# Kernel tuning notes

Measured on AMD Instinct MI355X. Metric: run time of the kernel, lower is better.

## Reference

```python
import jax, jax.numpy as jnp
import numpy as np

N = 8192
D = 1024
TIME_DECAY = 86400.0
EPS = 1e-10


def setup_inputs() -> dict:
    key = jax.random.key(0)
    ks = jax.random.split(key, 8)
    x = jax.random.normal(ks[0], (N, D), dtype=jnp.float32)
    # timestamps spanning ~10 days so decay bias is non-trivial
    timestamps = jax.random.uniform(ks[1], (N,), dtype=jnp.float32) * (10.0 * TIME_DECAY)
    s = 1.0 / np.sqrt(D)
    Wq = jax.random.normal(ks[2], (D, D), dtype=jnp.float32) * s
    bq = jnp.zeros((D,), dtype=jnp.float32)
    Wk = jax.random.normal(ks[3], (D, D), dtype=jnp.float32) * s
    bk = jnp.zeros((D,), dtype=jnp.float32)
    Wv = jax.random.normal(ks[4], (D, D), dtype=jnp.float32) * s
    bv = jnp.zeros((D,), dtype=jnp.float32)
    return {"x": x, "timestamps": timestamps, "Wq": Wq, "bq": bq,
            "Wk": Wk, "bk": bk, "Wv": Wv, "bv": bv}


def reference(x, timestamps, Wq, bq, Wk, bk, Wv, bv):
    scale = jnp.asarray(D ** 0.5, x.dtype)
    # torch nn.Linear: y = x @ W.T + b
    Q = x @ Wq.T + bq          # [N, D]
    K = x @ Wk.T + bk          # [N, D]
    V = x @ Wv.T + bv          # [N, D]
    time_diff = timestamps[:, None] - timestamps[None, :]   # [N, N]
    time_decay = jnp.exp(-jnp.abs(time_diff) / TIME_DECAY)  # [N, N]
    scores = (Q @ K.T) / scale + jnp.log(time_decay + EPS)  # [N, N]
    attn = jax.nn.softmax(scores, axis=-1)
    return attn @ V
```

## Files before the change

kernel.cpp:

```cpp
#include <hip/hip_runtime.h>


using half8   = __attribute__((ext_vector_type(8))) _Float16;
using half4   = __attribute__((ext_vector_type(4))) _Float16;
using floatx4 = __attribute__((ext_vector_type(4))) float;

__device__ __forceinline__ void gload_lds16(const void* g, void* l) {
  __builtin_amdgcn_global_load_lds((const __attribute__((address_space(1))) void*)g,
                                   (__attribute__((address_space(3))) void*)l,
                                   16, 0, 0);
}

template<int BIAS_MODE, int OUT_MODE, int SWZ>
__global__ __launch_bounds__(256)
void gemm64_k(const _Float16* __restrict__ A, const _Float16* __restrict__ B,
              void* __restrict__ Cout, const float* __restrict__ bias,
              int lda, int ldb, int ldc, int K, float outScale)
{
  __shared__ __align__(16) _Float16 As[128 * 64];
  __shared__ __align__(16) _Float16 Bs[128 * 64];
  const int tid = threadIdx.x;
  const int w = tid >> 6, lane = tid & 63;
  const int q = lane >> 4, l15 = lane & 15;
  const int wr = w >> 1, wc = w & 1;

  int tx, ty;
  if (SWZ) {
    const int bflat = blockIdx.y * gridDim.x + blockIdx.x;
    ty = bflat % gridDim.y;
    tx = bflat / gridDim.y;
  } else {
    tx = blockIdx.x; ty = blockIdx.y;
  }
  const long rowBase = (long)ty * 128;
  const long colBase = (long)tx * 128;

  const _Float16* Ag[4]; const _Float16* Bg[4];
  _Float16* Al[4]; _Float16* Bl[4];
#pragma unroll
  for (int p = 0; p < 4; ++p) {
    const int e = w * 2048 + p * 512 + lane * 8;
    const int row = e >> 6, c = (e >> 3) & 7;
    const int sc = (c ^ (row & 7)) << 3;
    Ag[p] = A + (rowBase + row) * lda + sc;
    Bg[p] = B + (colBase + row) * ldb + sc;
    Al[p] = &As[w * 2048 + p * 512];
    Bl[p] = &Bs[w * 2048 + p * 512];
  }

  floatx4 acc[4][4] = {};

  for (int k0 = 0; k0 < K; k0 += 64) {
    __syncthreads();
#pragma unroll
    for (int p = 0; p < 4; ++p) {
      gload_lds16(Ag[p], Al[p]);
      gload_lds16(Bg[p], Bl[p]);
      Ag[p] += 64; Bg[p] += 64;
    }
    __syncthreads();
#pragma unroll
    for (int kk = 0; kk < 2; ++kk) {
      half8 b[4];
#pragma unroll
      for (int j = 0; j < 4; ++j) {
        const int R = wc * 64 + 16 * j + l15;
        b[j] = *(const half8*)&Bs[R * 64 + (((kk * 4 + q) ^ (R & 7)) << 3)];
      }
#pragma unroll
      for (int i = 0; i < 4; ++i) {
        const int R = wr * 64 + 16 * i + l15;
        const half8 a = *(const half8*)&As[R * 64 + (((kk * 4 + q) ^ (R & 7)) << 3)];
#pragma unroll
        for (int j = 0; j < 4; ++j)
          acc[i][j] = __builtin_amdgcn_mfma_f32_16x16x32_f16(a, b[j], acc[i][j], 0, 0, 0);
      }
    }
  }

#pragma unroll
  for (int i = 0; i < 4; ++i) {
#pragma unroll
    for (int r = 0; r < 4; ++r) {
      const long rowg = rowBase + wr * 64 + 16 * i + q * 4 + r;
#pragma unroll
      for (int j = 0; j < 4; ++j) {
        const long colg = colBase + wc * 64 + 16 * j + l15;
        float v = acc[i][j][r];
        if (BIAS_MODE == 1) v += bias[colg];
        if (BIAS_MODE == 2) v += bias[rowg];
        if (BIAS_MODE == 3) v *= bias[rowg];
        v *= outScale;
        if (OUT_MODE == 2) ((float*)Cout)[rowg * ldc + colg] = v;
        else               ((_Float16*)Cout)[rowg * ldc + colg] = (_Float16)v;
      }
    }
  }
}

__global__ __launch_bounds__(256)
void gemm_stats_k(const _Float16* __restrict__ A, const _Float16* __restrict__ B,
                  const float* __restrict__ ts, _Float16* __restrict__ U,
                  float* __restrict__ part, int lda, int ldb, int N, int K,
                  float qkScale)
{
  __shared__ __align__(16) _Float16 As[128 * 64];
  __shared__ __align__(16) _Float16 Bs[128 * 64];
  __shared__ float trs[128], tcs[128];
  __shared__ float sL[2][2][64];
  const int tid = threadIdx.x;
  const int w = tid >> 6, lane = tid & 63;
  const int q = lane >> 4, l15 = lane & 15;
  const int wr = w >> 1, wc = w & 1;
  const long rowBase = (long)blockIdx.y * 128;
  const long colBase = (long)blockIdx.x * 128;

  if (tid < 128) {
    trs[tid] = ts[rowBase + tid];
    tcs[tid] = ts[colBase + tid];
  }

  const _Float16* Ag[4]; const _Float16* Bg[4];
  _Float16* Al[4]; _Float16* Bl[4];
#pragma unroll
  for (int p = 0; p < 4; ++p) {
    const int e = w * 2048 + p * 512 + lane * 8;
    const int row = e >> 6, c = (e >> 3) & 7;
    const int sc = (c ^ (row & 7)) << 3;
    Ag[p] = A + (rowBase + row) * lda + sc;
    Bg[p] = B + (colBase + row) * ldb + sc;
    Al[p] = &As[w * 2048 + p * 512];
    Bl[p] = &Bs[w * 2048 + p * 512];
  }

  floatx4 acc[4][4] = {};

  for (int k0 = 0; k0 < K; k0 += 64) {
    __syncthreads();
#pragma unroll
    for (int p = 0; p < 4; ++p) {
      gload_lds16(Ag[p], Al[p]);
      gload_lds16(Bg[p], Bl[p]);
      Ag[p] += 64; Bg[p] += 64;
    }
    __syncthreads();
#pragma unroll
    for (int kk = 0; kk < 2; ++kk) {
      half8 b[4];
#pragma unroll
      for (int j = 0; j < 4; ++j) {
        const int R = wc * 64 + 16 * j + l15;
        b[j] = *(const half8*)&Bs[R * 64 + (((kk * 4 + q) ^ (R & 7)) << 3)];
      }
#pragma unroll
      for (int i = 0; i < 4; ++i) {
        const int R = wr * 64 + 16 * i + l15;
        const half8 a = *(const half8*)&As[R * 64 + (((kk * 4 + q) ^ (R & 7)) << 3)];
#pragma unroll
        for (int j = 0; j < 4; ++j)
          acc[i][j] = __builtin_amdgcn_mfma_f32_16x16x32_f16(a, b[j], acc[i][j], 0, 0, 0);
      }
    }
  }

  const float inv_td = 1.0f / 86400.0f;
#pragma unroll
  for (int i = 0; i < 4; ++i) {
#pragma unroll
    for (int r = 0; r < 4; ++r) {
      const int rowl = wr * 64 + 16 * i + q * 4 + r;
      float ls = 0.0f;
#pragma unroll
      for (int j = 0; j < 4; ++j) {
        const int coll = wc * 64 + 16 * j + l15;
        const float sv = acc[i][j][r] * qkScale
                       - fabsf(trs[rowl] - tcs[coll]) * inv_td - 4.0f;
        const float u = __expf(sv);
        ls += u;
        U[(rowBase + rowl) * (long)N + (colBase + coll)] = (_Float16)u;
      }
      for (int mask = 1; mask <= 8; mask <<= 1)
        ls += __shfl_xor(ls, mask, 64);
      if (l15 == 0) sL[wr][wc][16 * i + 4 * q + r] = ls;
    }
  }
  __syncthreads();
  if (tid < 128) {
    const int wr2 = tid >> 6, rl = tid & 63;
    part[(rowBase + tid) * 64 + blockIdx.x] = sL[wr2][0][rl] + sL[wr2][1][rl];
  }
}

__global__ void combine_k(const float* __restrict__ part, float* __restrict__ invL) {
  const int r = blockIdx.x * 256 + threadIdx.x;
  float L = 0.0f;
  for (int c = 0; c < 64; ++c) L += part[(long)r * 64 + c];
  invL[r] = 1.0f / L;
}

__global__ void cvt_k(const float* __restrict__ in, _Float16* __restrict__ out, int n) {
  const int i = (blockIdx.x * 256 + threadIdx.x) * 4;
  if (i >= n) return;
  const float4 v = *(const float4*)(in + i);
  half4 o = { (_Float16)v.x, (_Float16)v.y, (_Float16)v.z, (_Float16)v.w };
  *(half4*)(out + i) = o;
}

extern "C" void kernel_launch(void* const* d_in, const int* in_sizes, int n_in,
                              void* d_out, int out_size, void* d_ws, size_t ws_size,
                              hipStream_t stream)
{
  (void)in_sizes; (void)n_in; (void)out_size; (void)ws_size;
  const int N = 8192, D = 1024;
  const float* x  = (const float*)d_in[0];
  const float* ts = (const float*)d_in[1];
  const float* Wq = (const float*)d_in[2];
  const float* bq = (const float*)d_in[3];
  const float* Wk = (const float*)d_in[4];
  const float* bk = (const float*)d_in[5];
  const float* Wv = (const float*)d_in[6];
  const float* bv = (const float*)d_in[7];

  char* p = (char*)d_ws;
  auto grab = [&](size_t bytes) {
    char* r = p;
    p += (bytes + 255) & ~(size_t)255;
    return r;
  };
  _Float16* xh    = (_Float16*)grab((size_t)N * D * 2);
  _Float16* wqkh  = (_Float16*)grab((size_t)2 * D * D * 2);
  _Float16* wvh   = (_Float16*)grab((size_t)D * D * 2);
  _Float16* QKcat = (_Float16*)grab((size_t)N * 2 * D * 2);
  _Float16* VTh   = (_Float16*)grab((size_t)D * N * 2);
  _Float16* Uh    = (_Float16*)grab((size_t)N * N * 2);
  float*    part  = (float*)grab((size_t)N * 64 * sizeof(float));
  float*    invL  = (float*)grab((size_t)N * sizeof(float));
  float*    bcat  = (float*)grab((size_t)2 * D * sizeof(float));

  cvt_k<<<N * D / 1024, 256, 0, stream>>>(x,  xh,  N * D);
  cvt_k<<<D * D / 1024, 256, 0, stream>>>(Wq, wqkh,         D * D);
  cvt_k<<<D * D / 1024, 256, 0, stream>>>(Wk, wqkh + D * D, D * D);
  cvt_k<<<D * D / 1024, 256, 0, stream>>>(Wv, wvh, D * D);
  hipMemcpyAsync(bcat,     bq, D * sizeof(float), hipMemcpyDeviceToDevice, stream);
  hipMemcpyAsync(bcat + D, bk, D * sizeof(float), hipMemcpyDeviceToDevice, stream);

  dim3 blk(256);
  gemm64_k<1, 0, 0><<<dim3(2 * D / 128, N / 128), blk, 0, stream>>>(
      xh, wqkh, QKcat, bcat, D, D, 2 * D, D, 1.0f);
  gemm64_k<2, 0, 0><<<dim3(N / 128, D / 128), blk, 0, stream>>>(
      wvh, xh, VTh, bv, D, D, N, D, 1.0f);
  gemm_stats_k<<<dim3(N / 128, N / 128), blk, 0, stream>>>(
      QKcat, QKcat + D, ts, Uh, part, 2 * D, 2 * D, N, D, 1.0f / 32.0f);
  combine_k<<<N / 256, 256, 0, stream>>>(part, invL);
  gemm64_k<3, 2, 1><<<dim3(D / 128, N / 128), blk, 0, stream>>>(
      Uh, VTh, d_out, invL, N, N, D, N, 1.0f);
}
```

Baseline: 513.9 us.

## Replace GEMMs with 256-tile, 512-thread kernels using a 4-stage LDS ring

All GEMM kernels are rewritten around a shared k-loop that keeps a 4-slot LDS ring of 32-wide K slices. Each step issues loads three slices ahead and waits with explicit vmcnt counts plus raw barriers, so global-to-LDS traffic overlaps MFMA work. Tiles grow to 256x256 or 256x128 with 8 waves per block, and MFMA sections are raised with setprio. The stats kernel uses 256x256 tiles, which halves the partial-sum columns consumed by combine_k. The trade-off is higher register and LDS pressure, fewer blocks per grid, and hand-counted waitcnt synchronisation that can go wrong.

```diff
diff --git a/kernel.cpp b/kernel.cpp
--- a/kernel.cpp
+++ b/kernel.cpp
@@ -11,18 +11,104 @@
                                    16, 0, 0);
 }
 
-template<int BIAS_MODE, int OUT_MODE, int SWZ>
-__global__ __launch_bounds__(256)
-void gemm64_k(const _Float16* __restrict__ A, const _Float16* __restrict__ B,
-              void* __restrict__ Cout, const float* __restrict__ bias,
-              int lda, int ldb, int ldc, int K, float outScale)
-{
-  __shared__ __align__(16) _Float16 As[128 * 64];
-  __shared__ __align__(16) _Float16 Bs[128 * 64];
+template<int N> __device__ __forceinline__ void waitv() {
+  if constexpr (N == 12)      asm volatile("s_waitcnt vmcnt(12)" ::: "memory");
+  else if constexpr (N == 9)  asm volatile("s_waitcnt vmcnt(9)"  ::: "memory");
+  else if constexpr (N == 8)  asm volatile("s_waitcnt vmcnt(8)"  ::: "memory");
+  else if constexpr (N == 6)  asm volatile("s_waitcnt vmcnt(6)"  ::: "memory");
+  else if constexpr (N == 4)  asm volatile("s_waitcnt vmcnt(4)"  ::: "memory");
+  else if constexpr (N == 3)  asm volatile("s_waitcnt vmcnt(3)"  ::: "memory");
+  else                        asm volatile("s_waitcnt vmcnt(0)"  ::: "memory");
+}
+
+template<int BM, int BN, int WM, int WN, int MI, int NJ>
+__device__ __forceinline__ void kloop_ring(
+    const _Float16* __restrict__ A, const _Float16* __restrict__ B,
+    long rowBase, long colBase, int lda, int ldb, int K,
+    _Float16* __restrict__ As, _Float16* __restrict__ Bs,
+    floatx4 (&acc)[MI][NJ])
+{
+  constexpr int LA = BM / 128, LB = BN / 128;
+  constexpr int ISS = LA + LB;
   const int tid = threadIdx.x;
   const int w = tid >> 6, lane = tid & 63;
   const int q = lane >> 4, l15 = lane & 15;
-  const int wr = w >> 1, wc = w & 1;
+  const int wr = w / WN, wcn = w & (WN - 1);
+
+  const int sc = (((lane & 3) ^ ((lane >> 3) & 3)) << 3);
+  const _Float16* Agp[LA]; int Aoff[LA];
+  const _Float16* Bgp[LB]; int Boff[LB];
+#pragma unroll
+  for (int p = 0; p < LA; ++p) {
+    const int row = ((w * (BM * 4) + p * 512 + lane * 8) >> 5);
+    Agp[p] = A + (rowBase + row) * (long)lda + sc;
+    Aoff[p] = w * (BM * 4) + p * 512;
+  }
+#pragma unroll
+  for (int p = 0; p < LB; ++p) {
+    const int row = ((w * (BN * 4) + p * 512 + lane * 8) >> 5);
+    Bgp[p] = B + (colBase + row) * (long)ldb + sc;
+    Boff[p] = w * (BN * 4) + p * 512;
+  }
+
+  const int pRd   = (q ^ ((l15 >> 1) & 3)) << 3;
+  const int aBase = (wr * (BM / WM) + l15) * 32 + pRd;
+  const int bBase = (wcn * (BN / WN) + l15) * 32 + pRd;
+
+  auto issue = [&](int t) {
+    const int s = t & 3;
+    const long ko = (long)t * 32;
+    _Float16* Asl = As + s * (BM * 32);
+    _Float16* Bsl = Bs + s * (BN * 32);
+#pragma unroll
+    for (int p = 0; p < LA; ++p) gload_lds16(Agp[p] + ko, Asl + Aoff[p]);
+#pragma unroll
+    for (int p = 0; p < LB; ++p) gload_lds16(Bgp[p] + ko, Bsl + Boff[p]);
+  };
+
+  auto compute = [&](int slot) {
+    const _Float16* Asl = As + slot * (BM * 32);
+    const _Float16* Bsl = Bs + slot * (BN * 32);
+    half8 bfr[NJ], afr[MI];
+#pragma unroll
+    for (int j = 0; j < NJ; ++j) bfr[j] = *(const half8*)&Bsl[bBase + j * 512];
+#pragma unroll
+    for (int i = 0; i < MI; ++i) afr[i] = *(const half8*)&Asl[aBase + i * 512];
+    __builtin_amdgcn_s_setprio(1);
+#pragma unroll
+    for (int i = 0; i < MI; ++i)
+#pragma unroll
+      for (int j = 0; j < NJ; ++j)
+        acc[i][j] = __builtin_amdgcn_mfma_f32_16x16x32_f16(afr[i], bfr[j], acc[i][j], 0, 0, 0);
+    __builtin_amdgcn_s_setprio(0);
+  };
+
+  const int NT = K >> 5;
+  issue(0); issue(1); issue(2);
+  for (int t = 0; t < NT - 3; ++t) {
+    issue(t + 3);
+    waitv<3 * ISS>();
+    __builtin_amdgcn_s_barrier();
+    compute(t & 3);
+    __builtin_amdgcn_s_barrier();
+  }
+  waitv<2 * ISS>(); __builtin_amdgcn_s_barrier();
+  compute((NT - 3) & 3);          __builtin_amdgcn_s_barrier();
+  waitv<1 * ISS>(); __builtin_amdgcn_s_barrier();
+  compute((NT - 2) & 3);          __builtin_amdgcn_s_barrier();
+  waitv<0>();       __builtin_amdgcn_s_barrier();
+  compute((NT - 1) & 3);
+}
+
+template<int BM, int BN, int WM, int WN, int BIAS_MODE, int OUT_MODE, int SWZ>
+__global__ __launch_bounds__(512, 2)
+void gemm256_k(const _Float16* __restrict__ A, const _Float16* __restrict__ B,
+               void* __restrict__ Cout, const float* __restrict__ bias,
+               int lda, int ldb, int ldc, int K, float outScale)
+{
+  constexpr int MI = BM / WM / 16, NJ = BN / WN / 16;
+  __shared__ __align__(16) _Float16 As[4 * BM * 32];
+  __shared__ __align__(16) _Float16 Bs[4 * BN * 32];
 
   int tx, ty;
   if (SWZ) {
@@ -32,60 +118,24 @@
   } else {
     tx = blockIdx.x; ty = blockIdx.y;
   }
-  const long rowBase = (long)ty * 128;
-  const long colBase = (long)tx * 128;
-
-  const _Float16* Ag[4]; const _Float16* Bg[4];
-  _Float16* Al[4]; _Float16* Bl[4];
-#pragma unroll
-  for (int p = 0; p < 4; ++p) {
-    const int e = w * 2048 + p * 512 + lane * 8;
-    const int row = e >> 6, c = (e >> 3) & 7;
-    const int sc = (c ^ (row & 7)) << 3;
-    Ag[p] = A + (rowBase + row) * lda + sc;
-    Bg[p] = B + (colBase + row) * ldb + sc;
-    Al[p] = &As[w * 2048 + p * 512];
-    Bl[p] = &Bs[w * 2048 + p * 512];
-  }
-
-  floatx4 acc[4][4] = {};
-
-  for (int k0 = 0; k0 < K; k0 += 64) {
-    __syncthreads();
-#pragma unroll
-    for (int p = 0; p < 4; ++p) {
-      gload_lds16(Ag[p], Al[p]);
-      gload_lds16(Bg[p], Bl[p]);
-      Ag[p] += 64; Bg[p] += 64;
-    }
-    __syncthreads();
-#pragma unroll
-    for (int kk = 0; kk < 2; ++kk) {
-      half8 b[4];
-#pragma unroll
-      for (int j = 0; j < 4; ++j) {
-        const int R = wc * 64 + 16 * j + l15;
-        b[j] = *(const half8*)&Bs[R * 64 + (((kk * 4 + q) ^ (R & 7)) << 3)];
-      }
-#pragma unroll
-      for (int i = 0; i < 4; ++i) {
-        const int R = wr * 64 + 16 * i + l15;
-        const half8 a = *(const half8*)&As[R * 64 + (((kk * 4 + q) ^ (R & 7)) << 3)];
-#pragma unroll
-        for (int j = 0; j < 4; ++j)
-          acc[i][j] = __builtin_amdgcn_mfma_f32_16x16x32_f16(a, b[j], acc[i][j], 0, 0, 0);
-      }
-    }
-  }
-
-#pragma unroll
-  for (int i = 0; i < 4; ++i) {
+  const long rowBase = (long)ty * BM;
+  const long colBase = (long)tx * BN;
+
+  floatx4 acc[MI][NJ] = {};
+  kloop_ring<BM, BN, WM, WN, MI, NJ>(A, B, rowBase, colBase, lda, ldb, K, As, Bs, acc);
+
+  const int tid = threadIdx.x;
+  const int w = tid >> 6, lane = tid & 63;
+  const int q = lane >> 4, l15 = lane & 15;
+  const int wr = w / WN, wcn = w & (WN - 1);
+#pragma unroll
+  for (int i = 0; i < MI; ++i) {
 #pragma unroll
     for (int r = 0; r < 4; ++r) {
-      const long rowg = rowBase + wr * 64 + 16 * i + q * 4 + r;
-#pragma unroll
-      for (int j = 0; j < 4; ++j) {
-        const long colg = colBase + wc * 64 + 16 * j + l15;
+      const long rowg = rowBase + wr * (BM / WM) + 16 * i + q * 4 + r;
+#pragma unroll
+      for (int j = 0; j < NJ; ++j) {
+        const long colg = colBase + wcn * (BN / WN) + 16 * j + l15;
         float v = acc[i][j][r];
         if (BIAS_MODE == 1) v += bias[colg];
         if (BIAS_MODE == 2) v += bias[rowg];
@@ -98,103 +148,66 @@
   }
 }
 
-__global__ __launch_bounds__(256)
-void gemm_stats_k(const _Float16* __restrict__ A, const _Float16* __restrict__ B,
-                  const float* __restrict__ ts, _Float16* __restrict__ U,
-                  float* __restrict__ part, int lda, int ldb, int N, int K,
-                  float qkScale)
-{
-  __shared__ __align__(16) _Float16 As[128 * 64];
-  __shared__ __align__(16) _Float16 Bs[128 * 64];
-  __shared__ float trs[128], tcs[128];
-  __shared__ float sL[2][2][64];
+__global__ __launch_bounds__(512, 2)
+void gemm_stats256_k(const _Float16* __restrict__ A, const _Float16* __restrict__ B,
+                     const float* __restrict__ ts, _Float16* __restrict__ U,
+                     float* __restrict__ part, int lda, int ldb, int N, int K,
+                     float qkScale)
+{
+  constexpr int BM = 256, BN = 256, WM = 2, WN = 4, MI = 8, NJ = 4;
+  __shared__ __align__(16) _Float16 As[4 * BM * 32];
+  __shared__ __align__(16) _Float16 Bs[4 * BN * 32];
+  __shared__ float trs[256], tcs[256];
+  __shared__ float sL[2][4][128];
   const int tid = threadIdx.x;
+  const long rowBase = (long)blockIdx.y * 256;
+  const long colBase = (long)blockIdx.x * 256;
+
+  if (tid < 256) {
+    trs[tid] = ts[rowBase + tid];
+    tcs[tid] = ts[colBase + tid];
+  }
+
+  floatx4 acc[MI][NJ] = {};
+  kloop_ring<BM, BN, WM, WN, MI, NJ>(A, B, rowBase, colBase, lda, ldb, K, As, Bs, acc);
+
   const int w = tid >> 6, lane = tid & 63;
   const int q = lane >> 4, l15 = lane & 15;
-  const int wr = w >> 1, wc = w & 1;
-  const long rowBase = (long)blockIdx.y * 128;
-  const long colBase = (long)blockIdx.x * 128;
-
-  if (tid < 128) {
-    trs[tid] = ts[rowBase + tid];
-    tcs[tid] = ts[colBase + tid];
-  }
-
-  const _Float16* Ag[4]; const _Float16* Bg[4];
-  _Float16* Al[4]; _Float16* Bl[4];
-#pragma unroll
-  for (int p = 0; p < 4; ++p) {
-    const int e = w * 2048 + p * 512 + lane * 8;
-    const int row = e >> 6, c = (e >> 3) & 7;
-    const int sc = (c ^ (row & 7)) << 3;
-    Ag[p] = A + (rowBase + row) * lda + sc;
-    Bg[p] = B + (colBase + row) * ldb + sc;
-    Al[p] = &As[w * 2048 + p * 512];
-    Bl[p] = &Bs[w * 2048 + p * 512];
-  }
-
-  floatx4 acc[4][4] = {};
-
-  for (int k0 = 0; k0 < K; k0 += 64) {
-    __syncthreads();
-#pragma unroll
-    for (int p = 0; p < 4; ++p) {
-      gload_lds16(Ag[p], Al[p]);
-      gload_lds16(Bg[p], Bl[p]);
-      Ag[p] += 64; Bg[p] += 64;
-    }
-    __syncthreads();
-#pragma unroll
-    for (int kk = 0; kk < 2; ++kk) {
-      half8 b[4];
+  const int wr = w >> 2, wcn = w & 3;
+  const float inv_td = 1.0f / 86400.0f;
+#pragma unroll
+  for (int i = 0; i < 8; ++i) {
+#pragma unroll
+    for (int r = 0; r < 4; ++r) {
+      const int rowl = wr * 128 + 16 * i + q * 4 + r;
+      const float tr = trs[rowl];
+      float ls = 0.0f;
 #pragma unroll
       for (int j = 0; j < 4; ++j) {
-        const int R = wc * 64 + 16 * j + l15;
-        b[j] = *(const half8*)&Bs[R * 64 + (((kk * 4 + q) ^ (R & 7)) << 3)];
-      }
-#pragma unroll
-      for (int i = 0; i < 4; ++i) {
-        const int R = wr * 64 + 16 * i + l15;
-        const half8 a = *(const half8*)&As[R * 64 + (((kk * 4 + q) ^ (R & 7)) << 3)];
-#pragma unroll
-        for (int j = 0; j < 4; ++j)
-          acc[i][j] = __builtin_amdgcn_mfma_f32_16x16x32_f16(a, b[j], acc[i][j], 0, 0, 0);
-      }
-    }
-  }
-
-  const float inv_td = 1.0f / 86400.0f;
-#pragma unroll
-  for (int i = 0; i < 4; ++i) {
-#pragma unroll
-    for (int r = 0; r < 4; ++r) {
-      const int rowl = wr * 64 + 16 * i + q * 4 + r;
-      float ls = 0.0f;
-#pragma unroll
-      for (int j = 0; j < 4; ++j) {
-        const int coll = wc * 64 + 16 * j + l15;
+        const int coll = wcn * 64 + 16 * j + l15;
         const float sv = acc[i][j][r] * qkScale
-                       - fabsf(trs[rowl] - tcs[coll]) * inv_td - 4.0f;
+                       - fabsf(tr - tcs[coll]) * inv_td - 4.0f;
         const float u = __expf(sv);
         ls += u;
         U[(rowBase + rowl) * (long)N + (colBase + coll)] = (_Float16)u;
       }
       for (int mask = 1; mask <= 8; mask <<= 1)
         ls += __shfl_xor(ls, mask, 64);
-      if (l15 == 0) sL[wr][wc][16 * i + 4 * q + r] = ls;
+      if (l15 == 0) sL[wr][wcn][16 * i + 4 * q + r] = ls;
     }
   }
   __syncthreads();
-  if (tid < 128) {
-    const int wr2 = tid >> 6, rl = tid & 63;
-    part[(rowBase + tid) * 64 + blockIdx.x] = sL[wr2][0][rl] + sL[wr2][1][rl];
+  if (tid < 256) {
+    const int wr2 = tid >> 7, rl = tid & 127;
+    part[(rowBase + tid) * 32 + blockIdx.x] =
+        sL[wr2][0][rl] + sL[wr2][1][rl] + sL[wr2][2][rl] + sL[wr2][3][rl];
   }
 }
 
 __global__ void combine_k(const float* __restrict__ part, float* __restrict__ invL) {
   const int r = blockIdx.x * 256 + threadIdx.x;
   float L = 0.0f;
-  for (int c = 0; c < 64; ++c) L += part[(long)r * 64 + c];
+  for (int c = 0; c < 32; ++c) L += part[(long)r * 32 + c];
   invL[r] = 1.0f / L;
 }
 
@@ -233,7 +246,7 @@
   _Float16* QKcat = (_Float16*)grab((size_t)N * 2 * D * 2);
   _Float16* VTh   = (_Float16*)grab((size_t)D * N * 2);
   _Float16* Uh    = (_Float16*)grab((size_t)N * N * 2);
-  float*    part  = (float*)grab((size_t)N * 64 * sizeof(float));
+  float*    part  = (float*)grab((size_t)N * 32 * sizeof(float));
   float*    invL  = (float*)grab((size_t)N * sizeof(float));
   float*    bcat  = (float*)grab((size_t)2 * D * sizeof(float));
 
@@ -244,14 +257,14 @@
   hipMemcpyAsync(bcat,     bq, D * sizeof(float), hipMemcpyDeviceToDevice, stream);
   hipMemcpyAsync(bcat + D, bk, D * sizeof(float), hipMemcpyDeviceToDevice, stream);
 
-  dim3 blk(256);
-  gemm64_k<1, 0, 0><<<dim3(2 * D / 128, N / 128), blk, 0, stream>>>(
+  dim3 blk(512);
+  gemm256_k<256, 256, 2, 4, 1, 0, 0><<<dim3(2 * D / 256, N / 256), blk, 0, stream>>>(
       xh, wqkh, QKcat, bcat, D, D, 2 * D, D, 1.0f);
-  gemm64_k<2, 0, 0><<<dim3(N / 128, D / 128), blk, 0, stream>>>(
+  gemm256_k<128, 256, 2, 4, 2, 0, 0><<<dim3(N / 256, D / 128), blk, 0, stream>>>(
       wvh, xh, VTh, bv, D, D, N, D, 1.0f);
-  gemm_stats_k<<<dim3(N / 128, N / 128), blk, 0, stream>>>(
+  gemm_stats256_k<<<dim3(N / 256, N / 256), blk, 0, stream>>>(
       QKcat, QKcat + D, ts, Uh, part, 2 * D, 2 * D, N, D, 1.0f / 32.0f);
   combine_k<<<N / 256, 256, 0, stream>>>(part, invL);
-  gemm64_k<3, 2, 1><<<dim3(D / 128, N / 128), blk, 0, stream>>>(
+  gemm256_k<256, 128, 4, 2, 3, 2, 1><<<dim3(D / 128, N / 256), blk, 0, stream>>>(
       Uh, VTh, d_out, invL, N, N, D, N, 1.0f);
 }
```

New measurement: 555.0 us. +8.0%, slower.
